# Performance work log

Measured on AMD Instinct MI355X. Metric: run time of the kernel, lower is better.

## Reference

```python
import jax, jax.numpy as jnp
import numpy as np

NUM_INPUT = 700
NUM_HIDDEN = 256
NUM_OUTPUT = 20
WIN = 50
BATCH = 512
DELAYS = (0, 16, 32)
MAX_D = 32
N_LAYERS = 2
THRESH = 0.3
ALPHA = 0.8  # membrane decay tau_m
LENS = 0.5   # surrogate-gradient window

@jax.custom_vjp
def spike_fn(u):
    # Heaviside with rectangular surrogate gradient (ActFun in the torch repo)
    return (u > 0.0).astype(u.dtype)

def _spike_fwd(u):
    return spike_fn(u), u

def _spike_bwd(u, g):
    return (g * (jnp.abs(u) < LENS).astype(u.dtype),)

spike_fn.defvjp(_spike_fwd, _spike_bwd)


def setup_inputs() -> dict:
    key = jax.random.key(0)
    ks = jax.random.split(key, 6)
    def init(k, shape, fan_in):
        return (jax.random.normal(k, shape, jnp.float32) / np.sqrt(fan_in)).astype(jnp.float32)
    return {
        "x":  jax.random.uniform(ks[0], (BATCH, WIN, NUM_INPUT), jnp.float32),
        # one input Linear per delay: [n_delays, H, In]
        "Wd": init(ks[1], (len(DELAYS), NUM_HIDDEN, NUM_INPUT), NUM_INPUT),
        "bd": jnp.zeros((len(DELAYS), NUM_HIDDEN), jnp.float32),
        # per-layer feedforward and recurrent weights
        "Wf": init(ks[2], (N_LAYERS, NUM_HIDDEN, NUM_HIDDEN), NUM_HIDDEN),
        "bf": jnp.zeros((N_LAYERS, NUM_HIDDEN), jnp.float32),
        "Wr": init(ks[3], (N_LAYERS, NUM_HIDDEN, NUM_HIDDEN), NUM_HIDDEN),
        # readout
        "Wo": init(ks[4], (NUM_OUTPUT, NUM_HIDDEN), NUM_HIDDEN),
        "bo": jnp.zeros((NUM_OUTPUT,), jnp.float32),
    }


def _forward(x, Wd, bd, Wf, bf, Wr, Wo, bo):
    B, win, _ = x.shape
    # extended_input: zeros for the first MAX_D steps, then the input
    ext = jnp.pad(x, ((0, 0), (MAX_D, 0), (0, 0)))
    # Precompute summed delayed input currents for all timesteps at once.
    cur = jnp.zeros((B, win, NUM_HIDDEN), x.dtype)
    for i, d in enumerate(DELAYS):
        sl = jax.lax.dynamic_slice_in_dim(ext, MAX_D - d, win, axis=1)
        cur = cur + jnp.einsum('bti,hi->bth', sl, Wd[i]) + bd[i]

    def step(carry, cur_t):
        mems, spks, o_mem, o_spk, o_sum, out_mot = carry
        prev = cur_t  # [B, H] summed delayed-input activations
        new_m, new_s = [], []
        for l in range(N_LAYERS):
            m = mems[l] * ALPHA * (1.0 - spks[l]) + prev @ Wf[l].T + bf[l] + spks[l] @ Wr[l].T
            s = spike_fn(m - THRESH)
            new_m.append(m)
            new_s.append(s)
            prev = s
        o_mem = o_mem * ALPHA * (1.0 - o_spk) + prev @ Wo.T + bo
        o_spk = spike_fn(o_mem - THRESH)
        o_sum = o_sum + o_spk
        out_mot = out_mot + jax.nn.softmax(o_mem, axis=1)
        return (jnp.stack(new_m), jnp.stack(new_s), o_mem, o_spk, o_sum, out_mot), None

    z = jnp.zeros((B, NUM_OUTPUT), x.dtype)
    zh = jnp.zeros((N_LAYERS, B, NUM_HIDDEN), x.dtype)
    carry0 = (zh, zh, z, z, z, z)
    carry, _ = jax.lax.scan(step, carry0, jnp.swapaxes(cur, 0, 1))
    _, _, _, _, o_sum, out_mot = carry
    return (o_sum / win, out_mot)


def reference(x, Wd, bd, Wf, bf, Wr, Wo, bo):
    return _forward(x, Wd, bd, Wf, bf, Wr, Wo, bo)
```

## Files before the change

### kernel.cpp

```cpp
#include <hip/hip_runtime.h>
#include <cstddef>

#define CUR_ELEMS (25600 * 256)
#define WROWS 65792

__global__ __launch_bounds__(256) void k0_transpose(
    const float* __restrict__ Wf, const float* __restrict__ Wr,
    const float* __restrict__ Wo, float* __restrict__ ws) {
  int tid = blockIdx.x * blockDim.x + threadIdx.x;
  float* Wr0T = ws + CUR_ELEMS;
  float* Wf1T = Wr0T + WROWS;
  float* Wr1T = Wf1T + WROWS;
  float* WoT  = Wr1T + WROWS;
  if (tid < WROWS) {
    int k = tid >> 8, h = tid & 255;
    Wr0T[tid] = (k < 256) ? Wr[h * 256 + k] : 0.f;
  } else if (tid < 2 * WROWS) {
    int i = tid - WROWS; int k = i >> 8, h = i & 255;
    Wf1T[i] = (k < 256) ? Wf[65536 + h * 256 + k] : 0.f;
  } else if (tid < 3 * WROWS) {
    int i = tid - 2 * WROWS; int k = i >> 8, h = i & 255;
    Wr1T[i] = (k < 256) ? Wr[65536 + h * 256 + k] : 0.f;
  } else if (tid < 3 * WROWS + 5140) {
    int i = tid - 3 * WROWS; int k = i / 20, j = i - k * 20;
    WoT[i] = (k < 256) ? Wo[j * 256 + k] : 0.f;
  }
}

__global__ __launch_bounds__(256) void k1_cur(
    const float* __restrict__ x, const float* __restrict__ Wd,
    const float* __restrict__ bd, float* __restrict__ cur) {
  __shared__ float As[2][16][132];
  __shared__ float Bs[2][16][132];
  const int tile = blockIdx.x & 7;
  const int u = blockIdx.x >> 3;
  const int bt = tile >> 1, ht = tile & 1;
  const int b0 = bt * 128, h0 = ht * 128;
  const int tid = threadIdx.x;
  const int tx = tid & 15, ty = tid >> 4;
  const int r = tid & 127, half = tid >> 7;
  const int kk0a = half * 8;

  int tJ[2], nJ[2];
  if (u < 6)       { tJ[0] = 32 + u;          nJ[0] = 3; tJ[1] = u;              nJ[1] = 1; }
  else if (u < 9)  { tJ[0] = 26 + 2 * (u - 6); nJ[0] = 2; tJ[1] = 27 + 2 * (u - 6); nJ[1] = 2; }
  else if (u < 21) { tJ[0] = 38 + (u - 9);    nJ[0] = 3; tJ[1] = 0;              nJ[1] = 0; }
  else             { tJ[0] = 16 + (u - 21);   nJ[0] = 2; tJ[1] = 6 + (u - 21);   nJ[1] = 1; }

  float bias[8];
#pragma unroll
  for (int q = 0; q < 2; ++q)
#pragma unroll
    for (int c = 0; c < 4; ++c) {
      const int col = h0 + q * 64 + tx * 4 + c;
      bias[q * 4 + c] = bd[col] + bd[256 + col] + bd[512 + col];
    }

  const int DEL[3] = {0, 16, 32};
#pragma unroll 1
  for (int jb = 0; jb < 2; ++jb) {
    const int npass = nJ[jb];
    if (npass == 0) continue;
    const int t = tJ[jb];

    float acc[8][8];
#pragma unroll
    for (int i = 0; i < 8; ++i)
#pragma unroll
      for (int j = 0; j < 8; ++j) acc[i][j] = 0.f;

#pragma unroll 1
    for (int di = 0; di < npass; ++di) {
      const int tsrc = t - DEL[di];
      const float* Arow = x + ((size_t)(b0 + r) * 50 + tsrc) * 700;
      const float* Brow = Wd + (size_t)di * 179200 + (size_t)(h0 + r) * 700;
      float4 pa0, pa1, pb0, pb1;
      pa0 = *(const float4*)(Arow + kk0a);
      pa1 = *(const float4*)(Arow + kk0a + 4);
      pb0 = *(const float4*)(Brow + kk0a);
      pb1 = *(const float4*)(Brow + kk0a + 4);
      As[0][kk0a + 0][r] = pa0.x; As[0][kk0a + 1][r] = pa0.y;
      As[0][kk0a + 2][r] = pa0.z; As[0][kk0a + 3][r] = pa0.w;
      As[0][kk0a + 4][r] = pa1.x; As[0][kk0a + 5][r] = pa1.y;
      As[0][kk0a + 6][r] = pa1.z; As[0][kk0a + 7][r] = pa1.w;
      Bs[0][kk0a + 0][r] = pb0.x; Bs[0][kk0a + 1][r] = pb0.y;
      Bs[0][kk0a + 2][r] = pb0.z; Bs[0][kk0a + 3][r] = pb0.w;
      Bs[0][kk0a + 4][r] = pb1.x; Bs[0][kk0a + 5][r] = pb1.y;
      Bs[0][kk0a + 6][r] = pb1.z; Bs[0][kk0a + 7][r] = pb1.w;
      pa0 = *(const float4*)(Arow + 16 + kk0a);
      pa1 = *(const float4*)(Arow + 16 + kk0a + 4);
      pb0 = *(const float4*)(Brow + 16 + kk0a);
      pb1 = *(const float4*)(Brow + 16 + kk0a + 4);
      __syncthreads();
#pragma unroll 1
      for (int c = 0; c < 44; ++c) {
        const int cb = c & 1, nb = cb ^ 1;
        if (c < 43) {
          As[nb][kk0a + 0][r] = pa0.x; As[nb][kk0a + 1][r] = pa0.y;
          As[nb][kk0a + 2][r] = pa0.z; As[nb][kk0a + 3][r] = pa0.w;
          As[nb][kk0a + 4][r] = pa1.x; As[nb][kk0a + 5][r] = pa1.y;
          As[nb][kk0a + 6][r] = pa1.z; As[nb][kk0a + 7][r] = pa1.w;
          Bs[nb][kk0a + 0][r] = pb0.x; Bs[nb][kk0a + 1][r] = pb0.y;
          Bs[nb][kk0a + 2][r] = pb0.z; Bs[nb][kk0a + 3][r] = pb0.w;
          Bs[nb][kk0a + 4][r] = pb1.x; Bs[nb][kk0a + 5][r] = pb1.y;
          Bs[nb][kk0a + 6][r] = pb1.z; Bs[nb][kk0a + 7][r] = pb1.w;
        }
        if (c < 42) {
          const int i0 = (c + 2) * 16 + kk0a, i1 = i0 + 4;
          pa0 = (i0 + 3 < 700) ? *(const float4*)(Arow + i0)
                               : make_float4(0.f, 0.f, 0.f, 0.f);
          pa1 = (i1 + 3 < 700) ? *(const float4*)(Arow + i1)
                               : make_float4(0.f, 0.f, 0.f, 0.f);
          pb0 = (i0 + 3 < 700) ? *(const float4*)(Brow + i0)
                               : make_float4(0.f, 0.f, 0.f, 0.f);
          pb1 = (i1 + 3 < 700) ? *(const float4*)(Brow + i1)
                               : make_float4(0.f, 0.f, 0.f, 0.f);
        }
#pragma unroll
        for (int kk = 0; kk < 16; ++kk) {
          const float4 a0 = *(const float4*)&As[cb][kk][ty * 4];
          const float4 a1 = *(const float4*)&As[cb][kk][64 + ty * 4];
          const float4 c0 = *(const float4*)&Bs[cb][kk][tx * 4];
          const float4 c1 = *(const float4*)&Bs[cb][kk][64 + tx * 4];
          const float ar[8] = {a0.x, a0.y, a0.z, a0.w, a1.x, a1.y, a1.z, a1.w};
          const float br[8] = {c0.x, c0.y, c0.z, c0.w, c1.x, c1.y, c1.z, c1.w};
#pragma unroll
          for (int rr = 0; rr < 8; ++rr)
#pragma unroll
            for (int cc = 0; cc < 8; ++cc) acc[rr][cc] += ar[rr] * br[cc];
        }
        __syncthreads();
      }
    }
#pragma unroll
    for (int p = 0; p < 2; ++p)
#pragma unroll
      for (int rr = 0; rr < 4; ++rr) {
        const int row = b0 + p * 64 + ty * 4 + rr;
        float* dst = cur + ((size_t)t * 512 + row) * 256 + h0;
        const int ai = p * 4 + rr;
        float4 v0 = make_float4(acc[ai][0] + bias[0], acc[ai][1] + bias[1],
                                acc[ai][2] + bias[2], acc[ai][3] + bias[3]);
        float4 v1 = make_float4(acc[ai][4] + bias[4], acc[ai][5] + bias[5],
                                acc[ai][6] + bias[6], acc[ai][7] + bias[7]);
        *(float4*)(dst + tx * 4) = v0;
        *(float4*)(dst + 64 + tx * 4) = v1;
      }
    __syncthreads();
  }
}

__global__ __launch_bounds__(256) void k1b_ff0(
    const float* __restrict__ Wf, const float* __restrict__ bf,
    float* __restrict__ cur) {
  __shared__ float As[16][68];
  __shared__ float Bs[16][260];
  const int m0 = blockIdx.x * 64;
  const int tid = threadIdx.x;
  const int tx = tid & 15, ty = tid >> 4;
  const int lr = tid & 63, akk = (tid >> 6) * 4;

  float acc[4][16];
#pragma unroll
  for (int i = 0; i < 4; ++i)
#pragma unroll
    for (int j = 0; j < 16; ++j) acc[i][j] = 0.f;

#pragma unroll 1
  for (int k0 = 0; k0 < 256; k0 += 16) {
    float4 av = *(const float4*)(cur + (size_t)(m0 + lr) * 256 + k0 + akk);
    As[akk + 0][lr] = av.x; As[akk + 1][lr] = av.y;
    As[akk + 2][lr] = av.z; As[akk + 3][lr] = av.w;
#pragma unroll
    for (int e = 0; e < 4; ++e) {
      const int hh = e * 64 + lr;
      float4 bv = *(const float4*)(Wf + (size_t)hh * 256 + k0 + akk);
      Bs[akk + 0][hh] = bv.x; Bs[akk + 1][hh] = bv.y;
      Bs[akk + 2][hh] = bv.z; Bs[akk + 3][hh] = bv.w;
    }
    __syncthreads();
#pragma unroll
    for (int kk = 0; kk < 16; ++kk) {
      const float4 a = *(const float4*)&As[kk][ty * 4];
      const float ar[4] = {a.x, a.y, a.z, a.w};
#pragma unroll
      for (int q = 0; q < 4; ++q) {
        const float4 bq = *(const float4*)&Bs[kk][q * 64 + tx * 4];
        const float br[4] = {bq.x, bq.y, bq.z, bq.w};
#pragma unroll
        for (int rr = 0; rr < 4; ++rr)
#pragma unroll
          for (int cc = 0; cc < 4; ++cc)
            acc[rr][q * 4 + cc] += ar[rr] * br[cc];
      }
    }
    __syncthreads();
  }
  float bias[16];
#pragma unroll
  for (int q = 0; q < 4; ++q)
#pragma unroll
    for (int c = 0; c < 4; ++c) bias[q * 4 + c] = bf[q * 64 + tx * 4 + c];
#pragma unroll
  for (int rr = 0; rr < 4; ++rr) {
    float* dst = cur + (size_t)(m0 + ty * 4 + rr) * 256;
#pragma unroll
    for (int q = 0; q < 4; ++q) {
      float4 v = make_float4(acc[rr][q * 4 + 0] + bias[q * 4 + 0],
                             acc[rr][q * 4 + 1] + bias[q * 4 + 1],
                             acc[rr][q * 4 + 2] + bias[q * 4 + 2],
                             acc[rr][q * 4 + 3] + bias[q * 4 + 3]);
      *(float4*)(dst + q * 64 + tx * 4) = v;
    }
  }
}

__device__ __forceinline__ void load8rows(const float* __restrict__ W,
                                          const int* LC, int j, int l4,
                                          float4* w) {
  const int4 a = *(const int4*)(LC + j);
  const int4 c = *(const int4*)(LC + j + 4);
  w[0] = *(const float4*)(W + a.x + l4);
  w[1] = *(const float4*)(W + a.y + l4);
  w[2] = *(const float4*)(W + a.z + l4);
  w[3] = *(const float4*)(W + a.w + l4);
  w[4] = *(const float4*)(W + c.x + l4);
  w[5] = *(const float4*)(W + c.y + l4);
  w[6] = *(const float4*)(W + c.z + l4);
  w[7] = *(const float4*)(W + c.w + l4);
}

__device__ __forceinline__ void add8rows(float4& acc, const float4* w) {
  float4 t0, t1, t2, t3;
  t0.x = w[0].x + w[1].x; t0.y = w[0].y + w[1].y; t0.z = w[0].z + w[1].z; t0.w = w[0].w + w[1].w;
  t1.x = w[2].x + w[3].x; t1.y = w[2].y + w[3].y; t1.z = w[2].z + w[3].z; t1.w = w[2].w + w[3].w;
  t2.x = w[4].x + w[5].x; t2.y = w[4].y + w[5].y; t2.z = w[4].z + w[5].z; t2.w = w[4].w + w[5].w;
  t3.x = w[6].x + w[7].x; t3.y = w[6].y + w[7].y; t3.z = w[6].z + w[7].z; t3.w = w[6].w + w[7].w;
  t0.x += t1.x; t0.y += t1.y; t0.z += t1.z; t0.w += t1.w;
  t2.x += t3.x; t2.y += t3.y; t2.z += t3.z; t2.w += t3.w;
  acc.x += t0.x + t2.x; acc.y += t0.y + t2.y;
  acc.z += t0.z + t2.z; acc.w += t0.w + t2.w;
}

__device__ __forceinline__ float4 gather_rows(const float* __restrict__ W,
                                              const int* LC, int n, int l4) {
  float4 acc = make_float4(0.f, 0.f, 0.f, 0.f);
  const int G = n >> 3;
  if (G == 0) return acc;
  float4 w0[8], w1[8], w2[8], w3[8];
  load8rows(W, LC, 0,  l4, w0);
  load8rows(W, LC, 8,  l4, w1);
  load8rows(W, LC, 16, l4, w2);
  load8rows(W, LC, 24, l4, w3);
  int g = 4;
  for (; g + 4 <= G; g += 4) {
    add8rows(acc, w0); load8rows(W, LC, (g + 0) * 8, l4, w0);
    add8rows(acc, w1); load8rows(W, LC, (g + 1) * 8, l4, w1);
    add8rows(acc, w2); load8rows(W, LC, (g + 2) * 8, l4, w2);
    add8rows(acc, w3); load8rows(W, LC, (g + 3) * 8, l4, w3);
  }
  add8rows(acc, w0); add8rows(acc, w1);
  add8rows(acc, w2); add8rows(acc, w3);
  return acc;
}

__device__ __forceinline__ void gather_dual(
    const float* __restrict__ WA, const int* LA, int nA,
    const float* __restrict__ WB, const int* LB, int nB, int l4,
    float4& accA, float4& accB) {
  const int GA = nA >> 3, GB = nB >> 3;
  float4 wa0[8], wa1[8], wb0[8], wb1[8];
  if (GA) { load8rows(WA, LA, 0, l4, wa0); load8rows(WA, LA, 8, l4, wa1); }
  if (GB) { load8rows(WB, LB, 0, l4, wb0); load8rows(WB, LB, 8, l4, wb1); }
  int ga = 0, gb = 0;
  while (ga + 4 <= GA && gb + 4 <= GB) {
    add8rows(accA, wa0); load8rows(WA, LA, (ga + 2) * 8, l4, wa0);
    add8rows(accB, wb0); load8rows(WB, LB, (gb + 2) * 8, l4, wb0);
    add8rows(accA, wa1); load8rows(WA, LA, (ga + 3) * 8, l4, wa1);
    add8rows(accB, wb1); load8rows(WB, LB, (gb + 3) * 8, l4, wb1);
    ga += 2; gb += 2;
  }
  if (GA) {
    while (ga + 4 <= GA) {
      add8rows(accA, wa0); load8rows(WA, LA, (ga + 2) * 8, l4, wa0);
      add8rows(accA, wa1); load8rows(WA, LA, (ga + 3) * 8, l4, wa1);
      ga += 2;
    }
    add8rows(accA, wa0); add8rows(accA, wa1);
  }
  if (GB) {
    while (gb + 4 <= GB) {
      add8rows(accB, wb0); load8rows(WB, LB, (gb + 2) * 8, l4, wb0);
      add8rows(accB, wb1); load8rows(WB, LB, (gb + 3) * 8, l4, wb1);
      gb += 2;
    }
    add8rows(accB, wb0); add8rows(accB, wb1);
  }
}

__device__ __forceinline__ float add8o(const float* w) {
  return ((w[0] + w[1]) + (w[2] + w[3])) + ((w[4] + w[5]) + (w[6] + w[7]));
}

__global__ __launch_bounds__(64, 1) void k2_scan(
    const float* __restrict__ ff0, const float* __restrict__ Wr0T,
    const float* __restrict__ Wf1T, const float* __restrict__ Wr1T,
    const float* __restrict__ WoT, const float* __restrict__ bf,
    const float* __restrict__ bo, float* __restrict__ out) {
  __shared__ __align__(16) int LC0[288];
  __shared__ __align__(16) int LC1[288];
  __shared__ __align__(16) int LCb[280];
  __shared__ float WoTl[5140];
  __shared__ float obuf[20];
  const int b = blockIdx.x;
  const int lane = threadIdx.x;
  const int l4 = lane * 4;
  const unsigned long long lb = (1ull << lane) - 1ull;

  for (int i = lane; i < 1285; i += 64)
    *(float4*)(WoTl + 4 * i) = *(const float4*)(WoT + 4 * i);

  float4 m0 = make_float4(0.f, 0.f, 0.f, 0.f), m1 = m0;
  float4 s0v = m0, s1v = m0;
  const float4 bf1v = *(const float4*)(bf + 256 + l4);
  float omem = 0.f, ospk = 0.f, osum = 0.f, omot = 0.f;
  const float bov = (lane < 20) ? bo[lane] : 0.f;
  const int ro = lane / 3, rc = lane - ro * 3;
  int n0 = 0, n1g = 0, n1r = 0;

  const float* ffp = ff0 + (size_t)b * 256 + l4;
  float4 ff = *(const float4*)ffp;

#pragma unroll 1
  for (int t = 0; t < 50; ++t) {
    float4 ffn = ff;
    if (t < 49) ffn = *(const float4*)(ffp + (size_t)(t + 1) * 131072);
    float4 g0 = make_float4(0.f, 0.f, 0.f, 0.f);
    float4 gB = make_float4(0.f, 0.f, 0.f, 0.f);
    gather_dual(Wr0T, LC0, n0, Wr1T, LC1, n1g, l4, g0, gB);
    {
      m0.x = m0.x * 0.8f * (1.f - s0v.x) + ff.x + g0.x;
      m0.y = m0.y * 0.8f * (1.f - s0v.y) + ff.y + g0.y;
      m0.z = m0.z * 0.8f * (1.f - s0v.z) + ff.z + g0.z;
      m0.w = m0.w * 0.8f * (1.f - s0v.w) + ff.w + g0.w;
      s0v.x = (m0.x - 0.3f > 0.f) ? 1.f : 0.f;
      s0v.y = (m0.y - 0.3f > 0.f) ? 1.f : 0.f;
      s0v.z = (m0.z - 0.3f > 0.f) ? 1.f : 0.f;
      s0v.w = (m0.w - 0.3f > 0.f) ? 1.f : 0.f;
    }
    {
      const float sv[4] = {s0v.x, s0v.y, s0v.z, s0v.w};
      int base = 0;
#pragma unroll
      for (int q = 0; q < 4; ++q) {
        const bool sp = sv[q] > 0.f;
        const unsigned long long mk = __ballot(sp);
        const int pos = base + (int)__popcll(mk & lb);
        if (sp) LC0[pos] = (l4 + q) << 8;
        base += (int)__popcll(mk);
      }
      const int pad = (-base) & 31;
      if (lane < pad) LC0[base + lane] = 256 << 8;
      n0 = base + pad;
    }
    {
      const float4 g1 = gather_rows(Wf1T, LC0, n0, l4);
      m1.x = m1.x * 0.8f * (1.f - s1v.x) + bf1v.x + g1.x + gB.x;
      m1.y = m1.y * 0.8f * (1.f - s1v.y) + bf1v.y + g1.y + gB.y;
      m1.z = m1.z * 0.8f * (1.f - s1v.z) + bf1v.z + g1.z + gB.z;
      m1.w = m1.w * 0.8f * (1.f - s1v.w) + bf1v.w + g1.w + gB.w;
      s1v.x = (m1.x - 0.3f > 0.f) ? 1.f : 0.f;
      s1v.y = (m1.y - 0.3f > 0.f) ? 1.f : 0.f;
      s1v.z = (m1.z - 0.3f > 0.f) ? 1.f : 0.f;
      s1v.w = (m1.w - 0.3f > 0.f) ? 1.f : 0.f;
    }
    {
      const float sv[4] = {s1v.x, s1v.y, s1v.z, s1v.w};
      int base = 0;
#pragma unroll
      for (int q = 0; q < 4; ++q) {
        const bool sp = sv[q] > 0.f;
        const unsigned long long mk = __ballot(sp);
        const int pos = base + (int)__popcll(mk & lb);
        if (sp) { LC1[pos] = (l4 + q) << 8; LCb[pos] = (l4 + q) * 20; }
        base += (int)__popcll(mk);
      }
      const int padg = (-base) & 31;
      if (lane < padg) LC1[base + lane] = 256 << 8;
      n1g = base + padg;
      const int rem = base % 24;
      const int padr = rem ? (24 - rem) : 0;
      if (lane < padr) LCb[base + lane] = 256 * 20;
      n1r = base + padr;
    }
    {
      float v = 0.f;
      if (lane < 60) {
        const int GR = n1r / 24;
        int j = rc;
        for (int g = 0; g < GR; ++g) {
          int idx[8]; float w[8];
#pragma unroll
          for (int u2 = 0; u2 < 8; ++u2) idx[u2] = LCb[j + 3 * u2];
#pragma unroll
          for (int u2 = 0; u2 < 8; ++u2) w[u2] = WoTl[idx[u2] + ro];
          v += add8o(w);
          j += 24;
        }
      }
      const float v1 = __shfl_down(v, 1);
      const float v2 = __shfl_down(v, 2);
      v += v1 + v2;
      if (rc == 0 && lane < 60) obuf[ro] = v;
      if (lane < 20) {
        const float oacc = bov + obuf[lane];
        omem = omem * 0.8f * (1.f - ospk) + oacc;
        ospk = (omem - 0.3f > 0.f) ? 1.f : 0.f;
        osum += ospk;
        obuf[lane] = omem;
      }
      if (lane < 20) {
        float ov[20];
#pragma unroll
        for (int j2 = 0; j2 < 20; ++j2) ov[j2] = obuf[j2];
        float mx = ov[0];
#pragma unroll
        for (int j2 = 1; j2 < 20; ++j2) mx = fmaxf(mx, ov[j2]);
        float sm = 0.f;
#pragma unroll
        for (int j2 = 0; j2 < 20; ++j2) sm += expf(ov[j2] - mx);
        omot += expf(omem - mx) / sm;
      }
    }
    ff = ffn;
  }
  if (lane < 20) {
    out[b * 20 + lane] = osum / 50.0f;
    out[10240 + b * 20 + lane] = omot;
  }
}

extern "C" void kernel_launch(void* const* d_in, const int* in_sizes, int n_in,
                              void* d_out, int out_size, void* d_ws, size_t ws_size,
                              hipStream_t stream) {
  const float* x  = (const float*)d_in[0];
  const float* Wd = (const float*)d_in[1];
  const float* bd = (const float*)d_in[2];
  const float* Wf = (const float*)d_in[3];
  const float* bf = (const float*)d_in[4];
  const float* Wr = (const float*)d_in[5];
  const float* Wo = (const float*)d_in[6];
  const float* bo = (const float*)d_in[7];
  float* out = (float*)d_out;
  float* ws  = (float*)d_ws;

  float* cur  = ws;
  float* Wr0T = ws + CUR_ELEMS;
  float* Wf1T = Wr0T + WROWS;
  float* Wr1T = Wf1T + WROWS;
  float* WoT  = Wr1T + WROWS;

  hipLaunchKernelGGL(k0_transpose, dim3(792), dim3(256), 0, stream, Wf, Wr, Wo, ws);
  hipLaunchKernelGGL(k1_cur, dim3(248), dim3(256), 0, stream, x, Wd, bd, cur);
  hipLaunchKernelGGL(k1b_ff0, dim3(400), dim3(256), 0, stream, Wf, bf, cur);
  hipLaunchKernelGGL(k2_scan, dim3(512), dim3(64), 0, stream, cur, Wr0T, Wf1T,
                     Wr1T, WoT, bf, bo, out);
}
```

Baseline: 850.0 us.

## Overlap readout with recurrent gathers and shrink spike-list padding to 8

```diff
diff --git a/kernel.cpp b/kernel.cpp
--- a/kernel.cpp
+++ b/kernel.cpp
@@ -242,60 +242,40 @@
   acc.z += t0.z + t2.z; acc.w += t0.w + t2.w;
 }
 
-__device__ __forceinline__ float4 gather_rows(const float* __restrict__ W,
-                                              const int* LC, int n, int l4) {
-  float4 acc = make_float4(0.f, 0.f, 0.f, 0.f);
+__device__ __forceinline__ float4 gather_split(const float* __restrict__ W,
+                                               const int* LC, int n, int l4) {
   const int G = n >> 3;
-  if (G == 0) return acc;
-  float4 w0[8], w1[8], w2[8], w3[8];
-  load8rows(W, LC, 0,  l4, w0);
-  load8rows(W, LC, 8,  l4, w1);
-  load8rows(W, LC, 16, l4, w2);
-  load8rows(W, LC, 24, l4, w3);
-  int g = 4;
-  for (; g + 4 <= G; g += 4) {
-    add8rows(acc, w0); load8rows(W, LC, (g + 0) * 8, l4, w0);
-    add8rows(acc, w1); load8rows(W, LC, (g + 1) * 8, l4, w1);
-    add8rows(acc, w2); load8rows(W, LC, (g + 2) * 8, l4, w2);
-    add8rows(acc, w3); load8rows(W, LC, (g + 3) * 8, l4, w3);
-  }
-  add8rows(acc, w0); add8rows(acc, w1);
-  add8rows(acc, w2); add8rows(acc, w3);
-  return acc;
-}
-
-__device__ __forceinline__ void gather_dual(
-    const float* __restrict__ WA, const int* LA, int nA,
-    const float* __restrict__ WB, const int* LB, int nB, int l4,
-    float4& accA, float4& accB) {
-  const int GA = nA >> 3, GB = nB >> 3;
+  float4 accA = make_float4(0.f, 0.f, 0.f, 0.f), accB = accA;
+  if (G == 0) return accA;
+  const int GH = (G + 1) >> 1;
+  const int GBn = G - GH;
   float4 wa0[8], wa1[8], wb0[8], wb1[8];
-  if (GA) { load8rows(WA, LA, 0, l4, wa0); load8rows(WA, LA, 8, l4, wa1); }
-  if (GB) { load8rows(WB, LB, 0, l4, wb0); load8rows(WB, LB, 8, l4, wb1); }
+  load8rows(W, LC, 0, l4, wa0);
+  if (GH > 1) load8rows(W, LC, 8, l4, wa1);
+  if (GBn > 0) load8rows(W, LC, GH * 8, l4, wb0);
+  if (GBn > 1) load8rows(W, LC, (GH + 1) * 8, l4, wb1);
   int ga = 0, gb = 0;
-  while (ga + 4 <= GA && gb + 4 <= GB) {
-    add8rows(accA, wa0); load8rows(WA, LA, (ga + 2) * 8, l4, wa0);
-    add8rows(accB, wb0); load8rows(WB, LB, (gb + 2) * 8, l4, wb0);
-    add8rows(accA, wa1); load8rows(WA, LA, (ga + 3) * 8, l4, wa1);
-    add8rows(accB, wb1); load8rows(WB, LB, (gb + 3) * 8, l4, wb1);
+  while (ga + 2 <= GH && gb + 2 <= GBn) {
+    add8rows(accA, wa0); if (ga + 2 < GH) load8rows(W, LC, (ga + 2) * 8, l4, wa0);
+    add8rows(accB, wb0); if (gb + 2 < GBn) load8rows(W, LC, (GH + gb + 2) * 8, l4, wb0);
+    add8rows(accA, wa1); if (ga + 3 < GH) load8rows(W, LC, (ga + 3) * 8, l4, wa1);
+    add8rows(accB, wb1); if (gb + 3 < GBn) load8rows(W, LC, (GH + gb + 3) * 8, l4, wb1);
     ga += 2; gb += 2;
   }
-  if (GA) {
-    while (ga + 4 <= GA) {
-      add8rows(accA, wa0); load8rows(WA, LA, (ga + 2) * 8, l4, wa0);
-      add8rows(accA, wa1); load8rows(WA, LA, (ga + 3) * 8, l4, wa1);
-      ga += 2;
-    }
-    add8rows(accA, wa0); add8rows(accA, wa1);
-  }
-  if (GB) {
-    while (gb + 4 <= GB) {
-      add8rows(accB, wb0); load8rows(WB, LB, (gb + 2) * 8, l4, wb0);
-      add8rows(accB, wb1); load8rows(WB, LB, (gb + 3) * 8, l4, wb1);
-      gb += 2;
-    }
-    add8rows(accB, wb0); add8rows(accB, wb1);
-  }
+  while (ga + 2 <= GH) {
+    add8rows(accA, wa0); if (ga + 2 < GH) load8rows(W, LC, (ga + 2) * 8, l4, wa0);
+    add8rows(accA, wa1); if (ga + 3 < GH) load8rows(W, LC, (ga + 3) * 8, l4, wa1);
+    ga += 2;
+  }
+  if (ga < GH) add8rows(accA, wa0);
+  while (gb + 2 <= GBn) {
+    add8rows(accB, wb0); if (gb + 2 < GBn) load8rows(W, LC, (GH + gb + 2) * 8, l4, wb0);
+    add8rows(accB, wb1); if (gb + 3 < GBn) load8rows(W, LC, (GH + gb + 3) * 8, l4, wb1);
+    gb += 2;
+  }
+  if (gb < GBn) add8rows(accB, wb0);
+  return make_float4(accA.x + accB.x, accA.y + accB.y,
+                     accA.z + accB.z, accA.w + accB.w);
 }
 
 __device__ __forceinline__ float add8o(const float* w) {
@@ -307,8 +287,8 @@
     const float* __restrict__ Wf1T, const float* __restrict__ Wr1T,
     const float* __restrict__ WoT, const float* __restrict__ bf,
     const float* __restrict__ bo, float* __restrict__ out) {
-  __shared__ __align__(16) int LC0[288];
-  __shared__ __align__(16) int LC1[288];
+  __shared__ __align__(16) int LC0[264];
+  __shared__ __align__(16) int LC1[264];
   __shared__ __align__(16) int LCb[280];
   __shared__ float WoTl[5140];
   __shared__ float obuf[20];
@@ -331,13 +311,81 @@
   const float* ffp = ff0 + (size_t)b * 256 + l4;
   float4 ff = *(const float4*)ffp;
 
+  auto do_readout = [&]() {
+    float v = 0.f;
+    if (lane < 60) {
+      const int GR = n1r / 24;
+      int j = rc;
+      for (int g = 0; g < GR; ++g) {
+        int idx[8]; float w[8];
+#pragma unroll
+        for (int u2 = 0; u2 < 8; ++u2) idx[u2] = LCb[j + 3 * u2];
+#pragma unroll
+        for (int u2 = 0; u2 < 8; ++u2) w[u2] = WoTl[idx[u2] + ro];
+        v += add8o(w);
+        j += 24;
+      }
+    }
+    const float v1 = __shfl_down(v, 1);
+    const float v2 = __shfl_down(v, 2);
+    v += v1 + v2;
+    if (rc == 0 && lane < 60) obuf[ro] = v;
+    if (lane < 20) {
+      const float oacc = bov + obuf[lane];
+      omem = omem * 0.8f * (1.f - ospk) + oacc;
+      ospk = (omem - 0.3f > 0.f) ? 1.f : 0.f;
+      osum += ospk;
+      obuf[lane] = omem;
+    }
+    if (lane < 20) {
+      float ov[20];
+#pragma unroll
+      for (int j2 = 0; j2 < 20; ++j2) ov[j2] = obuf[j2];
+      float mx = ov[0];
+#pragma unroll
+      for (int j2 = 1; j2 < 20; ++j2) mx = fmaxf(mx, ov[j2]);
+      float sm = 0.f;
+#pragma unroll
+      for (int j2 = 0; j2 < 20; ++j2) sm += expf(ov[j2] - mx);
+      omot += expf(omem - mx) / sm;
+    }
+  };
+
 #pragma unroll 1
   for (int t = 0; t < 50; ++t) {
     float4 ffn = ff;
     if (t < 49) ffn = *(const float4*)(ffp + (size_t)(t + 1) * 131072);
+    const int GA = n0 >> 3, GB = n1g >> 3;
+    float4 wa0[8], wa1[8], wb0[8], wb1[8];
+    if (GA > 0) load8rows(Wr0T, LC0, 0, l4, wa0);
+    if (GA > 1) load8rows(Wr0T, LC0, 8, l4, wa1);
+    if (GB > 0) load8rows(Wr1T, LC1, 0, l4, wb0);
+    if (GB > 1) load8rows(Wr1T, LC1, 8, l4, wb1);
+    if (t > 0) do_readout();
     float4 g0 = make_float4(0.f, 0.f, 0.f, 0.f);
     float4 gB = make_float4(0.f, 0.f, 0.f, 0.f);
-    gather_dual(Wr0T, LC0, n0, Wr1T, LC1, n1g, l4, g0, gB);
+    {
+      int ga = 0, gb = 0;
+      while (ga + 2 <= GA && gb + 2 <= GB) {
+        add8rows(g0, wa0); if (ga + 2 < GA) load8rows(Wr0T, LC0, (ga + 2) * 8, l4, wa0);
+        add8rows(gB, wb0); if (gb + 2 < GB) load8rows(Wr1T, LC1, (gb + 2) * 8, l4, wb0);
+        add8rows(g0, wa1); if (ga + 3 < GA) load8rows(Wr0T, LC0, (ga + 3) * 8, l4, wa1);
+        add8rows(gB, wb1); if (gb + 3 < GB) load8rows(Wr1T, LC1, (gb + 3) * 8, l4, wb1);
+        ga += 2; gb += 2;
+      }
+      while (ga + 2 <= GA) {
+        add8rows(g0, wa0); if (ga + 2 < GA) load8rows(Wr0T, LC0, (ga + 2) * 8, l4, wa0);
+        add8rows(g0, wa1); if (ga + 3 < GA) load8rows(Wr0T, LC0, (ga + 3) * 8, l4, wa1);
+        ga += 2;
+      }
+      if (ga < GA) add8rows(g0, wa0);
+      while (gb + 2 <= GB) {
+        add8rows(gB, wb0); if (gb + 2 < GB) load8rows(Wr1T, LC1, (gb + 2) * 8, l4, wb0);
+        add8rows(gB, wb1); if (gb + 3 < GB) load8rows(Wr1T, LC1, (gb + 3) * 8, l4, wb1);
+        gb += 2;
+      }
+      if (gb < GB) add8rows(gB, wb0);
+    }
     {
       m0.x = m0.x * 0.8f * (1.f - s0v.x) + ff.x + g0.x;
       m0.y = m0.y * 0.8f * (1.f - s0v.y) + ff.y + g0.y;
@@ -359,12 +407,12 @@
         if (sp) LC0[pos] = (l4 + q) << 8;
         base += (int)__popcll(mk);
       }
-      const int pad = (-base) & 31;
+      const int pad = (-base) & 7;
       if (lane < pad) LC0[base + lane] = 256 << 8;
       n0 = base + pad;
     }
     {
-      const float4 g1 = gather_rows(Wf1T, LC0, n0, l4);
+      const float4 g1 = gather_split(Wf1T, LC0, n0, l4);
       m1.x = m1.x * 0.8f * (1.f - s1v.x) + bf1v.x + g1.x + gB.x;
       m1.y = m1.y * 0.8f * (1.f - s1v.y) + bf1v.y + g1.y + gB.y;
       m1.z = m1.z * 0.8f * (1.f - s1v.z) + bf1v.z + g1.z + gB.z;
@@ -385,7 +433,7 @@
         if (sp) { LC1[pos] = (l4 + q) << 8; LCb[pos] = (l4 + q) * 20; }
         base += (int)__popcll(mk);
       }
-      const int padg = (-base) & 31;
+      const int padg = (-base) & 7;
       if (lane < padg) LC1[base + lane] = 256 << 8;
       n1g = base + padg;
       const int rem = base % 24;
@@ -393,47 +441,9 @@
       if (lane < padr) LCb[base + lane] = 256 * 20;
       n1r = base + padr;
     }
-    {
-      float v = 0.f;
-      if (lane < 60) {
-        const int GR = n1r / 24;
-        int j = rc;
-        for (int g = 0; g < GR; ++g) {
-          int idx[8]; float w[8];
-#pragma unroll
-          for (int u2 = 0; u2 < 8; ++u2) idx[u2] = LCb[j + 3 * u2];
-#pragma unroll
-          for (int u2 = 0; u2 < 8; ++u2) w[u2] = WoTl[idx[u2] + ro];
-          v += add8o(w);
-          j += 24;
-        }
-      }
-      const float v1 = __shfl_down(v, 1);
-      const float v2 = __shfl_down(v, 2);
-      v += v1 + v2;
-      if (rc == 0 && lane < 60) obuf[ro] = v;
-      if (lane < 20) {
-        const float oacc = bov + obuf[lane];
-        omem = omem * 0.8f * (1.f - ospk) + oacc;
-        ospk = (omem - 0.3f > 0.f) ? 1.f : 0.f;
-        osum += ospk;
-        obuf[lane] = omem;
-      }
-      if (lane < 20) {
-        float ov[20];
-#pragma unroll
-        for (int j2 = 0; j2 < 20; ++j2) ov[j2] = obuf[j2];
-        float mx = ov[0];
-#pragma unroll
-        for (int j2 = 1; j2 < 20; ++j2) mx = fmaxf(mx, ov[j2]);
-        float sm = 0.f;
-#pragma unroll
-        for (int j2 = 0; j2 < 20; ++j2) sm += expf(ov[j2] - mx);
-        omot += expf(omem - mx) / sm;
-      }
-    }
     ff = ffn;
   }
+  do_readout();
   if (lane < 20) {
     out[b * 20 + lane] = osum / 50.0f;
     out[10240 + b * 20 + lane] = omot;
```

Measured after the change: 972.1 us. +14.4%, slower.
